# Optimization experiments

Measured on AMD Instinct MI355X. Metric: run time of the kernel, lower is better.

The kernel has to match this reference:

```python
import jax, jax.numpy as jnp
import numpy as np

NB, T, N, C = 8, 8, 6890, 128
CLASS_NUM = 7
D_SUM = 512
PCADIM = 64
V = 7702  # garment template vertex count
EPS = 1e-5


def setup_inputs() -> dict:
    key = jax.random.key(0)
    ks = jax.random.split(key, 12)
    f = lambda k, s: jax.random.normal(k, s, dtype=jnp.float32)
    return {
        "x": f(ks[0], (NB, T, N, 3)),
        "sem_logits": f(ks[1], (NB * T, N, CLASS_NUM)),
        "feature": f(ks[2], (NB * T, C, N)),
        "garment_summary": f(ks[3], (NB, T, D_SUM)),
        "W1": f(ks[4], (128, D_SUM)) * 0.02, "b1": jnp.zeros((128,), jnp.float32),
        "g1": jnp.ones((128,), jnp.float32), "be1": jnp.zeros((128,), jnp.float32),
        "rm1": jnp.zeros((128,), jnp.float32), "rv1": jnp.ones((128,), jnp.float32),
        "W2": f(ks[5], (64, 128)) * 0.02, "b2": jnp.zeros((64,), jnp.float32),
        "g2": jnp.ones((64,), jnp.float32), "be2": jnp.zeros((64,), jnp.float32),
        "rm2": jnp.zeros((64,), jnp.float32), "rv2": jnp.ones((64,), jnp.float32),
        "W3": f(ks[6], (PCADIM, 64)) * 0.02, "b3": jnp.zeros((PCADIM,), jnp.float32),
        "pca_comp": f(ks[7], (PCADIM, V * 3)) * 0.02,
        "pca_mean": f(ks[8], (V * 3,)) * 0.02,
        "pca_scale": jnp.abs(f(ks[9], (V * 3,))) + 0.5,
        "garment_label": 1,
        "n": N // 4,
    }


def _segmentation_gather(x, sem_logits, feature, garment_label, n):
    # Vectorized form of the per-sample boolean-mask select / truncate / zero-pad loop.
    # x: [B,N,3]; feature: [B,C,N]; sem_logits: [B,N,K]
    feat = jnp.swapaxes(feature, 1, 2)                     # [B,N,C]
    labels = jnp.argmax(sem_logits, axis=2)                # [B,N] (detached in original)
    mask = labels == garment_label                         # [B,N]
    count = mask.sum(axis=1)                               # [B]
    # stable argsort puts selected (mask=True -> key False=0) indices first, in order
    order = jnp.argsort(jnp.logical_not(mask), axis=1)[:, :n]   # [B,n]
    valid = (jnp.arange(n)[None, :] < count[:, None]).astype(x.dtype)  # [B,n]
    gv = jnp.take_along_axis(x, order[:, :, None], axis=1) * valid[:, :, None]
    gf = jnp.take_along_axis(feat, order[:, :, None], axis=1) * valid[:, :, None]
    return gv, gf


def reference(x, sem_logits, feature, garment_summary, W1, b1, g1, be1, rm1, rv1,
              W2, b2, g2, be2, rm2, rv2, W3, b3, pca_comp, pca_mean, pca_scale,
              garment_label, n):
    nbatch, t = x.shape[0], x.shape[1]
    xf = x.reshape(nbatch * t, -1, 3)
    garment_v, garment_f = _segmentation_gather(xf, sem_logits, feature, garment_label, n)

    # PCAEncoder: 1x1 Conv1d over a length-1 sequence == linear layers; BN in eval mode
    def bn(h, g, be, rm, rv):
        return (h - rm) * jax.lax.rsqrt(rv + EPS) * g + be

    gs = garment_summary.max(axis=1)                       # [nbatch, 512] (max over T)
    h = jax.nn.relu(bn(gs @ W1.T + b1, g1, be1, rm1, rv1))
    h = jax.nn.relu(bn(h @ W2.T + b2, g2, be2, rm2, rv2))
    coeff = h @ W3.T + b3                                  # [nbatch, PCADIM]

    # PCA_inverse_transform
    tpose = ((coeff @ pca_comp) + pca_mean) * pca_scale
    tpose = tpose.reshape(coeff.shape[0], -1, 3)           # [nbatch, V, 3]
    return garment_v, garment_f, coeff, tpose
```

## Files before the change

### kernel.cpp

```cpp
#include <hip/hip_runtime.h>

#define NBATCH   8
#define TT       8
#define NPTS     6890
#define KCLS     7
#define CCH      128
#define BSAMP    64
#define NOUT     1722
#define DSUM     512
#define PCADIM   64
#define V3       23106
#define EPSBN    1e-5f

#define NW       108
#define PCH      128
#define CHB      2
#define CHN      64
#define LDSQ     129
#define CPG      9
#define NGRP     6
#define K4B      91
#define NSCAN    BSAMP
#define NGATHER  (BSAMP * CHB * NGRP)

#define OFF_GV     0
#define OFF_GF     (BSAMP * NOUT * 3)
#define OFF_COEFF  (OFF_GF + BSAMP * NOUT * CCH)
#define OFF_TPOSE  (OFF_COEFF + NBATCH * PCADIM)

__global__ __launch_bounds__(256) void k1_mask_mlp(
    const float* __restrict__ logits,
    const int*   __restrict__ d_label,
    unsigned long long* __restrict__ ws_mask,
    const float* __restrict__ gsum,
    const float* __restrict__ W1, const float* __restrict__ b1,
    const float* __restrict__ g1, const float* __restrict__ be1,
    const float* __restrict__ rm1, const float* __restrict__ rv1,
    const float* __restrict__ W2, const float* __restrict__ b2,
    const float* __restrict__ g2, const float* __restrict__ be2,
    const float* __restrict__ rm2, const float* __restrict__ rv2,
    const float* __restrict__ W3, const float* __restrict__ b3,
    float* __restrict__ coeff_out, float* __restrict__ coeff_ws)
{
    const int tid = threadIdx.x;

    if (blockIdx.x < BSAMP * 27) {
        const int b     = blockIdx.x / 27;
        const int chunk = blockIdx.x % 27;
        const int i     = chunk * 256 + tid;
        const int label = d_label[0];

        bool sel = false;
        if (i < NPTS) {
            const float* p = logits + ((size_t)b * NPTS + i) * KCLS;
            float best = p[0]; int bi = 0;
            #pragma unroll
            for (int k = 1; k < KCLS; ++k) {
                float v = p[k];
                if (v > best) { best = v; bi = k; }
            }
            sel = (bi == label);
        }
        const unsigned long long m = __ballot(sel);
        if ((tid & 63) == 0) {
            const int w = chunk * 4 + (tid >> 6);
            if (w < NW) ws_mask[b * NW + w] = m;
        }
    } else {
        const int s    = blockIdx.x - BSAMP * 27;
        const int lane = tid & 63;
        const int wv   = tid >> 6;

        __shared__ float gs[DSUM];
        __shared__ float h1[128];
        __shared__ float h2[64];

        for (int d = tid; d < DSUM; d += 256) {
            const float* p = gsum + ((size_t)s * TT) * DSUM + d;
            float m = p[0];
            #pragma unroll
            for (int t = 1; t < TT; ++t) m = fmaxf(m, p[(size_t)t * DSUM]);
            gs[d] = m;
        }
        __syncthreads();

        for (int r = 0; r < 32; r += 2) {
            const int j0 = wv * 32 + r, j1 = j0 + 1;
            const float* w0 = W1 + (size_t)j0 * DSUM;
            const float* w1 = W1 + (size_t)j1 * DSUM;
            float pa = 0.f, pb = 0.f;
            #pragma unroll
            for (int d = lane; d < DSUM; d += 64) {
                const float gd = gs[d];
                pa = fmaf(w0[d], gd, pa);
                pb = fmaf(w1[d], gd, pb);
            }
            #pragma unroll
            for (int off = 32; off; off >>= 1) {
                pa += __shfl_xor(pa, off);
                pb += __shfl_xor(pb, off);
            }
            if (lane == 0) {
                pa += b1[j0];
                pa = (pa - rm1[j0]) * rsqrtf(rv1[j0] + EPSBN) * g1[j0] + be1[j0];
                h1[j0] = fmaxf(pa, 0.f);
                pb += b1[j1];
                pb = (pb - rm1[j1]) * rsqrtf(rv1[j1] + EPSBN) * g1[j1] + be1[j1];
                h1[j1] = fmaxf(pb, 0.f);
            }
        }
        __syncthreads();

        for (int r = 0; r < 16; ++r) {
            const int jj = wv * 16 + r;
            const float* w = W2 + (size_t)jj * 128;
            float p = w[lane] * h1[lane] + w[lane + 64] * h1[lane + 64];
            #pragma unroll
            for (int off = 32; off; off >>= 1) p += __shfl_xor(p, off);
            if (lane == 0) {
                p += b2[jj];
                p = (p - rm2[jj]) * rsqrtf(rv2[jj] + EPSBN) * g2[jj] + be2[jj];
                h2[jj] = fmaxf(p, 0.f);
            }
        }
        __syncthreads();

        for (int r = 0; r < 16; ++r) {
            const int jj = wv * 16 + r;
            float p = W3[(size_t)jj * 64 + lane] * h2[lane];
            #pragma unroll
            for (int off = 32; off; off >>= 1) p += __shfl_xor(p, off);
            if (lane == 0) {
                p += b3[jj];
                coeff_out[s * PCADIM + jj] = p;
                coeff_ws[s * PCADIM + jj]  = p;
            }
        }
    }
}

__global__ __launch_bounds__(256, 4) void k2_all(
    const float* __restrict__ feature,
    const unsigned long long* __restrict__ ws_mask,
    const float* __restrict__ x,
    float* __restrict__ gv,
    float* __restrict__ gf,
    const float* __restrict__ coeff_ws,
    const float* __restrict__ comp,
    const float* __restrict__ mean_,
    const float* __restrict__ scale_,
    float* __restrict__ tpose)
{
    __shared__ float lds[CHN * LDSQ];
    __shared__ unsigned long long smask[NW];
    __shared__ int  swc[NW];
    __shared__ int  spos[PCH];
    __shared__ int  sel_list[PCH];
    __shared__ int  s_ns[2];
    __shared__ int  s_cnt;

    const int tid = threadIdx.x;

    if (blockIdx.x < K4B) {
        float* sc = lds;
        for (int o = tid; o < NBATCH * PCADIM; o += 256) sc[o] = coeff_ws[o];
        __syncthreads();

        const int v = blockIdx.x * 256 + tid;
        if (v >= V3) return;

        float acc[NBATCH];
        #pragma unroll
        for (int s = 0; s < NBATCH; ++s) acc[s] = 0.f;
        for (int k = 0; k < PCADIM; ++k) {
            const float pv = comp[(size_t)k * V3 + v];
            #pragma unroll
            for (int s = 0; s < NBATCH; ++s)
                acc[s] = fmaf(sc[s * PCADIM + k], pv, acc[s]);
        }
        const float mn = mean_[v], scl = scale_[v];
        #pragma unroll
        for (int s = 0; s < NBATCH; ++s)
            tpose[(size_t)s * V3 + v] = (acc[s] + mn) * scl;
        return;
    }

    if (blockIdx.x < K4B + NSCAN) {
        const int b = blockIdx.x - K4B;

        if (tid < NW) smask[tid] = ws_mask[b * NW + tid];
        __syncthreads();
        if (tid < NW) swc[tid] = __popcll(smask[tid]);
        __syncthreads();
        if (tid == 0) {
            int run = 0;
            for (int w = 0; w < NW; ++w) { int t = swc[w]; swc[w] = run; run += t; }
            s_cnt = run < NOUT ? run : NOUT;
        }
        __syncthreads();

        const float* xb = x + (size_t)b * NPTS * 3;
        for (int i = tid; i < NPTS; i += 256) {
            const int w = i >> 6, lb6 = i & 63;
            const unsigned long long m = smask[w];
            if ((m >> lb6) & 1ull) {
                const int pos = swc[w] + __popcll(m & ((1ull << lb6) - 1ull));
                if (pos < NOUT) {
                    const size_t go = ((size_t)b * NOUT + pos) * 3;
                    gv[go + 0] = xb[(size_t)i * 3 + 0];
                    gv[go + 1] = xb[(size_t)i * 3 + 1];
                    gv[go + 2] = xb[(size_t)i * 3 + 2];
                }
            }
        }
        for (int j = s_cnt + tid; j < NOUT; j += 256) {
            float* gp = gv + ((size_t)b * NOUT + j) * 3;
            gp[0] = 0.f; gp[1] = 0.f; gp[2] = 0.f;
        }
        return;
    }

    const int gb  = blockIdx.x - (K4B + NSCAN);
    const int b   = gb / (CHB * NGRP);
    const int rem = gb % (CHB * NGRP);
    const int cb  = rem / NGRP;
    const int g   = rem % NGRP;

    const int lane = tid & 63;
    const int cg   = tid >> 6;
    const int p0   = lane * 2;
    const float* fbase = feature + ((size_t)b * CCH + cb * CHN) * NPTS;

    float2 rc[16], rn[16];

    {
        const int i0 = g * (CPG * PCH);
        const int il = min(PCH, NPTS - i0);
        const float* fb = fbase + i0 + p0;
        if (p0 < il) {
            #pragma unroll
            for (int it = 0; it < 16; ++it)
                rc[it] = *(const float2*)(fb + (size_t)(cg * 16 + it) * NPTS);
        } else {
            #pragma unroll
            for (int it = 0; it < 16; ++it) rc[it] = make_float2(0.f, 0.f);
        }
    }

    if (tid < NW) smask[tid] = ws_mask[b * NW + tid];
    __syncthreads();
    if (tid < NW) swc[tid] = __popcll(smask[tid]);
    __syncthreads();
    if (tid == 0) {
        int run = 0;
        for (int w = 0; w < NW; ++w) { int t = swc[w]; swc[w] = run; run += t; }
        s_cnt = run < NOUT ? run : NOUT;
    }
    __syncthreads();

    {
        const int cnt  = s_cnt;
        const int tail = NOUT - cnt;
        if (tail > 0) {
            const int nshares = CHB * NGRP;
            const int share = (tail + nshares - 1) / nshares;
            const int idx   = cb * NGRP + g;
            const int r0    = cnt + idx * share;
            const int r1    = min(r0 + share, NOUT);
            const int nrows = r1 - r0;
            if (nrows > 0) {
                float4* base4 = (float4*)(gf + ((size_t)b * NOUT + r0) * CCH);
                const int total = nrows * 32;
                for (int f = tid; f < total; f += 256)
                    base4[f] = make_float4(0.f, 0.f, 0.f, 0.f);
            }
        }
    }

    #pragma unroll 1
    for (int c = 0; c < CPG; ++c) {
        const int chunk = g * CPG + c;

        if (c + 1 < CPG) {
            const int i1 = (chunk + 1) * PCH;
            const int il = min(PCH, NPTS - i1);
            const float* fb = fbase + i1 + p0;
            if (p0 < il) {
                #pragma unroll
                for (int it = 0; it < 16; ++it)
                    rn[it] = *(const float2*)(fb + (size_t)(cg * 16 + it) * NPTS);
            } else {
                #pragma unroll
                for (int it = 0; it < 16; ++it) rn[it] = make_float2(0.f, 0.f);
            }
        }

        __syncthreads();

        #pragma unroll
        for (int it = 0; it < 16; ++it) {
            const int cch = cg * 16 + it;
            lds[cch * LDSQ + p0]     = rc[it].x;
            lds[cch * LDSQ + p0 + 1] = rc[it].y;
        }

        if (tid < 128) {
            const int w    = tid >> 6;
            const int word = 2 * chunk + w;
            const unsigned long long m = smask[word];
            const int base = swc[word];
            const int sel  = (int)((m >> lane) & 1ull);
            const int pos  = base + __popcll(m & ((1ull << lane) - 1ull));
            const int sp   = (sel && pos < NOUT) ? pos : -1;
            spos[tid] = sp;
            const unsigned long long mm = __ballot(sp >= 0);
            const int before = __popcll(mm & ((1ull << lane) - 1ull));
            if (sp >= 0) sel_list[w * 64 + before] = tid;
            if (lane == 0) s_ns[w] = __popcll(mm);
        }
        __syncthreads();

        const int rw = tid >> 6;
        #pragma unroll 1
        for (int w = 0; w < 2; ++w) {
            const int ns = s_ns[w];
            for (int s = rw; s < ns; s += 4) {
                const int p   = sel_list[w * 64 + s];
                const int pos = spos[p];
                gf[((size_t)b * NOUT + pos) * CCH + cb * CHN + lane] =
                    lds[lane * LDSQ + p];
            }
        }

        if (c + 1 < CPG) {
            #pragma unroll
            for (int it = 0; it < 16; ++it) rc[it] = rn[it];
        }
    }
}

extern "C" void kernel_launch(void* const* d_in, const int* in_sizes, int n_in,
                              void* d_out, int out_size, void* d_ws, size_t ws_size,
                              hipStream_t stream) {
    const float* x      = (const float*)d_in[0];
    const float* logits = (const float*)d_in[1];
    const float* feat   = (const float*)d_in[2];
    const float* gsum   = (const float*)d_in[3];
    const float* W1  = (const float*)d_in[4];
    const float* b1  = (const float*)d_in[5];
    const float* g1  = (const float*)d_in[6];
    const float* be1 = (const float*)d_in[7];
    const float* rm1 = (const float*)d_in[8];
    const float* rv1 = (const float*)d_in[9];
    const float* W2  = (const float*)d_in[10];
    const float* b2  = (const float*)d_in[11];
    const float* g2  = (const float*)d_in[12];
    const float* be2 = (const float*)d_in[13];
    const float* rm2 = (const float*)d_in[14];
    const float* rv2 = (const float*)d_in[15];
    const float* W3  = (const float*)d_in[16];
    const float* b3  = (const float*)d_in[17];
    const float* comp  = (const float*)d_in[18];
    const float* mean_ = (const float*)d_in[19];
    const float* scale_= (const float*)d_in[20];
    const int* d_label = (const int*)d_in[21];

    float* out   = (float*)d_out;
    float* gv    = out + OFF_GV;
    float* gf    = out + OFF_GF;
    float* coeff = out + OFF_COEFF;
    float* tpose = out + OFF_TPOSE;

    unsigned long long* ws_mask = (unsigned long long*)d_ws;
    float* coeff_ws = (float*)(ws_mask + BSAMP * NW);

    k1_mask_mlp<<<BSAMP * 27 + NBATCH, 256, 0, stream>>>(
        logits, d_label, ws_mask, gsum, W1, b1, g1, be1, rm1, rv1,
        W2, b2, g2, be2, rm2, rv2, W3, b3, coeff, coeff_ws);

    k2_all<<<K4B + NSCAN + NGATHER, 256, 0, stream>>>(
        feat, ws_mask, x, gv, gf, coeff_ws, comp, mean_, scale_, tpose);
}
```

Measured before the change: 93.84 us.

## Retile feature gather to 256-point chunks of 32 channels with float4 loads

Reshapes the feature-gather tiling from 128-point by 64-channel chunks to 256-point by 32-channel chunks, so each lane loads float4 instead of float2 and writes float4 rows into LDS. All four wavefronts now build selection lists, one mask word each, and each wave writes its own selected points, with two points per wave instruction at 32 channels. The number of gather blocks stays the same. The change aims for wider global loads and less serial work per block, but the output writes per point become 128-byte segments instead of 256-byte ones. The LDS row padding of 260 may bring back bank conflicts on the column reads.

```diff
diff --git a/kernel.cpp b/kernel.cpp
--- a/kernel.cpp
+++ b/kernel.cpp
@@ -13,12 +13,12 @@
 #define EPSBN    1e-5f
 
 #define NW       108
-#define PCH      128
-#define CHB      2
-#define CHN      64
-#define LDSQ     129
+#define PCH      256
+#define CHB      4
+#define CHN      32
+#define LDSR     260
 #define CPG      9
-#define NGRP     6
+#define NGRP     3
 #define K4B      91
 #define NSCAN    BSAMP
 #define NGATHER  (BSAMP * CHB * NGRP)
@@ -151,12 +151,12 @@
     const float* __restrict__ scale_,
     float* __restrict__ tpose)
 {
-    __shared__ float lds[CHN * LDSQ];
+    __shared__ float lds[CHN * LDSR];
     __shared__ unsigned long long smask[NW];
     __shared__ int  swc[NW];
     __shared__ int  spos[PCH];
     __shared__ int  sel_list[PCH];
-    __shared__ int  s_ns[2];
+    __shared__ int  s_ns[4];
     __shared__ int  s_cnt;
 
     const int tid = threadIdx.x;
@@ -227,23 +227,29 @@
     const int g   = rem % NGRP;
 
     const int lane = tid & 63;
-    const int cg   = tid >> 6;
-    const int p0   = lane * 2;
+    const int wv   = tid >> 6;
+    const int p4   = lane * 4;
     const float* fbase = feature + ((size_t)b * CCH + cb * CHN) * NPTS;
 
-    float2 rc[16], rn[16];
+    float4 rc[8], rn[8];
 
     {
-        const int i0 = g * (CPG * PCH);
+        const int i0 = (g * CPG) * PCH;
         const int il = min(PCH, NPTS - i0);
-        const float* fb = fbase + i0 + p0;
-        if (p0 < il) {
-            #pragma unroll
-            for (int it = 0; it < 16; ++it)
-                rc[it] = *(const float2*)(fb + (size_t)(cg * 16 + it) * NPTS);
+        const float* fb = fbase + i0 + p4;
+        if (p4 + 4 <= il) {
+            #pragma unroll
+            for (int it = 0; it < 8; ++it)
+                rc[it] = *(const float4*)(fb + (size_t)(wv * 8 + it) * NPTS);
+        } else if (p4 < il) {
+            #pragma unroll
+            for (int it = 0; it < 8; ++it) {
+                float2 v = *(const float2*)(fb + (size_t)(wv * 8 + it) * NPTS);
+                rc[it] = make_float4(v.x, v.y, 0.f, 0.f);
+            }
         } else {
             #pragma unroll
-            for (int it = 0; it < 16; ++it) rc[it] = make_float2(0.f, 0.f);
+            for (int it = 0; it < 8; ++it) rc[it] = make_float4(0.f, 0.f, 0.f, 0.f);
         }
     }
 
@@ -284,57 +290,62 @@
         if (c + 1 < CPG) {
             const int i1 = (chunk + 1) * PCH;
             const int il = min(PCH, NPTS - i1);
-            const float* fb = fbase + i1 + p0;
-            if (p0 < il) {
+            const float* fb = fbase + i1 + p4;
+            if (p4 + 4 <= il) {
                 #pragma unroll
-                for (int it = 0; it < 16; ++it)
-                    rn[it] = *(const float2*)(fb + (size_t)(cg * 16 + it) * NPTS);
+                for (int it = 0; it < 8; ++it)
+                    rn[it] = *(const float4*)(fb + (size_t)(wv * 8 + it) * NPTS);
+            } else if (p4 < il) {
+                #pragma unroll
+                for (int it = 0; it < 8; ++it) {
+                    float2 v = *(const float2*)(fb + (size_t)(wv * 8 + it) * NPTS);
+                    rn[it] = make_float4(v.x, v.y, 0.f, 0.f);
+                }
             } else {
                 #pragma unroll
-                for (int it = 0; it < 16; ++it) rn[it] = make_float2(0.f, 0.f);
+                for (int it = 0; it < 8; ++it) rn[it] = make_float4(0.f, 0.f, 0.f, 0.f);
             }
         }
 
         __syncthreads();
 
         #pragma unroll
-        for (int it = 0; it < 16; ++it) {
-            const int cch = cg * 16 + it;
-            lds[cch * LDSQ + p0]     = rc[it].x;
-            lds[cch * LDSQ + p0 + 1] = rc[it].y;
-        }
-
-        if (tid < 128) {
-            const int w    = tid >> 6;
-            const int word = 2 * chunk + w;
+        for (int it = 0; it < 8; ++it) {
+            const int r = wv * 8 + it;
+            *(float4*)(&lds[r * LDSR + p4]) = rc[it];
+        }
+
+        {
+            const int word = 4 * chunk + wv;
             const unsigned long long m = smask[word];
             const int base = swc[word];
             const int sel  = (int)((m >> lane) & 1ull);
             const int pos  = base + __popcll(m & ((1ull << lane) - 1ull));
             const int sp   = (sel && pos < NOUT) ? pos : -1;
-            spos[tid] = sp;
+            const int plocal = wv * 64 + lane;
+            spos[plocal] = sp;
             const unsigned long long mm = __ballot(sp >= 0);
             const int before = __popcll(mm & ((1ull << lane) - 1ull));
-            if (sp >= 0) sel_list[w * 64 + before] = tid;
-            if (lane == 0) s_ns[w] = __popcll(mm);
-        }
-        __syncthreads();
-
-        const int rw = tid >> 6;
-        #pragma unroll 1
-        for (int w = 0; w < 2; ++w) {
-            const int ns = s_ns[w];
-            for (int s = rw; s < ns; s += 4) {
-                const int p   = sel_list[w * 64 + s];
+            if (sp >= 0) sel_list[wv * 64 + before] = plocal;
+            if (lane == 0) s_ns[wv] = __popcll(mm);
+        }
+        __syncthreads();
+
+        {
+            const int ns   = s_ns[wv];
+            const int half = lane >> 5;
+            const int ch   = lane & 31;
+            for (int s = half; s < ns; s += 2) {
+                const int p   = sel_list[wv * 64 + s];
                 const int pos = spos[p];
-                gf[((size_t)b * NOUT + pos) * CCH + cb * CHN + lane] =
-                    lds[lane * LDSQ + p];
+                gf[((size_t)b * NOUT + pos) * CCH + cb * CHN + ch] =
+                    lds[ch * LDSR + p];
             }
         }
 
         if (c + 1 < CPG) {
             #pragma unroll
-            for (int it = 0; it < 16; ++it) rc[it] = rn[it];
+            for (int it = 0; it < 8; ++it) rc[it] = rn[it];
         }
     }
 }
```

Result: faster. 90.04 us (-4.0%).
